# Kernel optimization log

Hardware: AMD Instinct MI355X
Metric: run time of the kernel (lower is better)

## Reference

```python
import jax, jax.numpy as jnp
import numpy as np

S, B, D, H, OUT = 512, 200, 64, 256, 3  # B == window_len - 2 = 200
EPS = 1e-5


def setup_inputs() -> dict:
    key = jax.random.key(0)
    ks = jax.random.split(key, 16)
    f = lambda k, sh, s=0.05: jax.random.normal(k, sh, dtype=jnp.float32) * s
    return {
        "x": f(ks[0], (S, B, D), 1.0),
        "w_ih0": f(ks[1], (3 * H, D)), "w_hh0": f(ks[2], (3 * H, H)),
        "b_ih0": f(ks[3], (3 * H,)), "b_hh0": f(ks[4], (3 * H,)),
        "w_ih1": f(ks[5], (3 * H, H)), "w_hh1": f(ks[6], (3 * H, H)),
        "b_ih1": f(ks[7], (3 * H,)), "b_hh1": f(ks[8], (3 * H,)),
        "ln_w": jnp.ones((H,), jnp.float32), "ln_b": jnp.zeros((H,), jnp.float32),
        "fc2_w": f(ks[9], (512, B * H), 0.01), "fc2_b": f(ks[10], (512,)),
        "bn_g": jnp.ones((512,), jnp.float32), "bn_b": jnp.zeros((512,), jnp.float32),
        "fc3_w": f(ks[11], (OUT, 512)), "fc3_b": f(ks[12], (OUT,)),
    }


def _gru_layer(x, w_ih, w_hh, b_ih, b_hh):
    # x: (S, B, D_in) -> (S, B, H), torch nn.GRU gate order [r, z, n]
    gi = jnp.einsum('sbd,gd->sbg', x, w_ih) + b_ih  # precompute input gates
    h0 = jnp.zeros((x.shape[1], w_hh.shape[1]), x.dtype)

    def step(h, gi_t):
        gh = h @ w_hh.T + b_hh
        ir, iz, inn = jnp.split(gi_t, 3, axis=-1)
        hr, hz, hn = jnp.split(gh, 3, axis=-1)
        r = jax.nn.sigmoid(ir + hr)
        z = jax.nn.sigmoid(iz + hz)
        n = jnp.tanh(inn + r * hn)
        h_new = (1.0 - z) * n + z * h
        return h_new, h_new

    _, hs = jax.lax.scan(step, h0, gi)
    return hs


def reference(x, w_ih0, w_hh0, b_ih0, b_hh0, w_ih1, w_hh1, b_ih1, b_hh1,
              ln_w, ln_b, fc2_w, fc2_b, bn_g, bn_b, fc3_w, fc3_b):
    h = _gru_layer(x, w_ih0, w_hh0, b_ih0, b_hh0)
    h = _gru_layer(h, w_ih1, w_hh1, b_ih1, b_hh1)
    # LayerNorm over hidden dim, then ReLU
    mu = jnp.mean(h, axis=-1, keepdims=True)
    var = jnp.var(h, axis=-1, keepdims=True)
    h = (h - mu) * jax.lax.rsqrt(var + EPS) * ln_w + ln_b
    h = jax.nn.relu(h)
    # flatten: (S, B*H)
    h = h.reshape(h.shape[0], -1)
    y = h @ fc2_w.T + fc2_b
    # BatchNorm1d (training mode: batch stats over axis 0, biased var)
    mu2 = jnp.mean(y, axis=0)
    var2 = jnp.var(y, axis=0)
    y = (y - mu2) * jax.lax.rsqrt(var2 + EPS) * bn_g + bn_b
    y = jax.nn.relu(y)
    return y @ fc3_w.T + fc3_b
```

## Files before the change

### kernel.cpp

```cpp
#include <hip/hip_runtime.h>
#include <stdint.h>

typedef _Float16 f16;
typedef _Float16 f16x4 __attribute__((ext_vector_type(4)));
typedef _Float16 f16x8 __attribute__((ext_vector_type(8)));
typedef float f32x4 __attribute__((ext_vector_type(4)));

#define SEQ 512
#define NB  200
#define HD  256
#define GD  768
#define BW  16
#define NBLK 13
#define GI_TSTRIDE (NBLK*4*6*512)
#define LOG2E 1.44269504f

__device__ __forceinline__ f32x4 mfma16(f16x8 a, f16x8 b, f32x4 c){
  return __builtin_amdgcn_mfma_f32_16x16x32_f16(a, b, c, 0, 0, 0);
}

__global__ void cvt_f32_f16(const float* __restrict__ src, f16* __restrict__ dst, int n4){
  int i = blockIdx.x * blockDim.x + threadIdx.x;
  int stride = gridDim.x * blockDim.x;
  for (; i < n4; i += stride){
    float4 v = ((const float4*)src)[i];
    f16x4 o = { (f16)v.x, (f16)v.y, (f16)v.z, (f16)v.w };
    ((f16x4*)dst)[i] = o;
  }
}

template<int MODE>
__global__ __launch_bounds__(256, 2)
void gemm_bt(const f16* __restrict__ A, const f16* __restrict__ B,
             f16* __restrict__ Cb, float* __restrict__ Cf,
             const float* __restrict__ bias1, const float* __restrict__ bias2,
             int K, int N, int klen)
{
  const int l  = threadIdx.x & 63;
  const int w  = threadIdx.x >> 6;
  const int lr = l & 15, lg = l >> 4;
  const int Mb = blockIdx.x * 128 + (w >> 1) * 64;
  const int Nb = blockIdx.y * 128 + (w & 1) * 64;
  const int kb = blockIdx.z * klen;

  const f16* Ap = A + (size_t)(Mb + lr) * K + kb + lg * 8;
  const f16* Bp = B + (size_t)(Nb + lr) * K + kb + lg * 8;

  f32x4 acc[4][4];
  #pragma unroll
  for (int i = 0; i < 4; ++i)
    #pragma unroll
    for (int j = 0; j < 4; ++j)
      acc[i][j] = (f32x4){0.f, 0.f, 0.f, 0.f};

  for (int k = 0; k < klen; k += 32){
    f16x8 af[4], bfr[4];
    #pragma unroll
    for (int i = 0; i < 4; ++i){
      af[i]  = *(const f16x8*)(Ap + (size_t)i * 16 * K + k);
      bfr[i] = *(const f16x8*)(Bp + (size_t)i * 16 * K + k);
    }
    #pragma unroll
    for (int i = 0; i < 4; ++i)
      #pragma unroll
      for (int j = 0; j < 4; ++j)
        acc[i][j] = mfma16(af[i], bfr[j], acc[i][j]);
  }

  if (MODE == 0){
    float bv[4];
    #pragma unroll
    for (int j = 0; j < 4; ++j){
      int g = Nb + j*16 + lr;
      bv[j] = bias1[g] + (g < 512 ? bias2[g] : 0.f);
    }
    #pragma unroll
    for (int i = 0; i < 4; ++i)
      #pragma unroll
      for (int r = 0; r < 4; ++r){
        int row = Mb + i*16 + lg*4 + r;
        int t = (int)(((uint64_t)(uint32_t)row * 167773u) >> 25);
        int b = row - t*200;
        int bblk = b >> 4, blr = b & 15;
        #pragma unroll
        for (int j = 0; j < 4; ++j){
          int g = Nb + j*16 + lr;
          int q = g >> 8, jr = g & 255;
          int ww = jr >> 6, t4 = (jr >> 4) & 3, lg2 = (jr >> 2) & 3, rr = g & 3;
          size_t idx = ((((size_t)(t*13 + bblk)*4 + ww)*6 + (q*2 + (t4>>1)))*64
                        + lg2*16 + blr)*8 + (t4&1)*4 + rr;
          Cb[idx] = (f16)(acc[i][j][r] + bv[j]);
        }
      }
  } else {
    #pragma unroll
    for (int i = 0; i < 4; ++i)
      #pragma unroll
      for (int j = 0; j < 4; ++j)
        #pragma unroll
        for (int r = 0; r < 4; ++r){
          int row = Mb + i*16 + lg*4 + r;
          int col = Nb + j*16 + lr;
          Cf[((size_t)blockIdx.z * 512 + row) * N + col] = acc[i][j][r];
        }
  }
}

__global__
__attribute__((amdgpu_flat_work_group_size(256, 256), amdgpu_waves_per_eu(1, 1)))
void gru_layer(const f16* __restrict__ whh, const float* __restrict__ bhh,
               const f16* __restrict__ gi, f16* __restrict__ hs)
{
  __shared__ __align__(16) unsigned char sm[16384 + 49152 + 24576];
  const int tid = threadIdx.x;
  const int w  = tid >> 6, l = tid & 63;
  const int lr = l & 15, lg = l >> 4;
  const int b0 = blockIdx.x * BW;
  const bool bval = (b0 + lr) < NB;

  ((int4*)sm)[tid]       = make_int4(0,0,0,0);
  ((int4*)sm)[tid + 256] = make_int4(0,0,0,0);

  const f16* glane = gi + ((size_t)(blockIdx.x*4 + w))*6*512 + l*8;
#define DMA_GI(P) do { \
    _Pragma("unroll") \
    for (int c = 0; c < 6; ++c) \
      __builtin_amdgcn_global_load_lds( \
          (const __attribute__((address_space(1))) void*)(glane + c*512), \
          (__attribute__((address_space(3))) void*)(sm + 16384 + (P)*24576 + w*6144 + c*1024), \
          16, 0, 0); \
  } while(0)

  DMA_GI(0);

  f16x8 wA[12][8];
  #pragma unroll
  for (int q = 0; q < 3; ++q)
    #pragma unroll
    for (int t4 = 0; t4 < 4; ++t4)
      #pragma unroll
      for (int kk = 0; kk < 8; ++kk)
        wA[q*4+t4][kk] = *(const f16x8*)(whh + (size_t)(q*256 + w*64 + t4*16 + lr)*256 + kk*32 + lg*8);

  f16x4 bn[4];
  #pragma unroll
  for (int t4 = 0; t4 < 4; ++t4){
    float4 bv = *(const float4*)(bhh + 512 + w*64 + t4*16 + lg*4);
    bn[t4] = (f16x4){(f16)bv.x,(f16)bv.y,(f16)bv.z,(f16)bv.w};
  }

  const int cswz = ((lr ^ (lr >> 2)) & 3) << 4;
  const int hrd = lr*64 + ((lg*16) ^ cswz);
  const int girdb = 16384 + w*6144 + l*16;

  f16* hp = hs + (size_t)(b0 + lr)*HD + w*64 + lg*4;
  f16x4 hvp[4];
  #pragma unroll
  for (int t4 = 0; t4 < 4; ++t4) hvp[t4] = (f16x4){(f16)0.f,(f16)0.f,(f16)0.f,(f16)0.f};

  asm volatile("s_waitcnt vmcnt(0)" ::: "memory");
  __syncthreads();

#define GRUSTEP(P) do { \
    asm volatile("s_waitcnt vmcnt(4)" ::: "memory");  \
    f16x8 c0 = *(const f16x8*)(sm + (P)*24576 + girdb + 0*1024); \
    f16x8 c1 = *(const f16x8*)(sm + (P)*24576 + girdb + 1*1024); \
    f16x8 c2 = *(const f16x8*)(sm + (P)*24576 + girdb + 2*1024); \
    f16x8 c3 = *(const f16x8*)(sm + (P)*24576 + girdb + 3*1024); \
    f16x8 innA = *(const f16x8*)(sm + (P)*24576 + girdb + 4*1024); \
    f16x8 innB = *(const f16x8*)(sm + (P)*24576 + girdb + 5*1024); \
    f32x4 acc[12]; \
    _Pragma("unroll") \
    for (int t4 = 0; t4 < 4; ++t4){ \
      _Pragma("unroll") \
      for (int r = 0; r < 4; ++r){ \
        acc[0*4+t4][r] = (float)((t4 < 2 ? c0 : c1)[(t4&1)*4 + r]); \
        acc[1*4+t4][r] = (float)((t4 < 2 ? c2 : c3)[(t4&1)*4 + r]); \
        acc[2*4+t4][r] = (float)(bn[t4][r]); \
      } \
    } \
    glane += GI_TSTRIDE; \
    DMA_GI((P)^1); \
    _Pragma("unroll") \
    for (int kk = 0; kk < 8; ++kk){ \
      f16x8 hf = *(const f16x8*)(sm + (P)*8192 + kk*1024 + hrd); \
      _Pragma("unroll") \
      for (int i = 0; i < 12; ++i) \
        acc[i] = mfma16(wA[i][kk], hf, acc[i]); \
    } \
    _Pragma("unroll") \
    for (int t4 = 0; t4 < 4; ++t4){ \
      f16x4 hv; \
      _Pragma("unroll") \
      for (int r = 0; r < 4; ++r){ \
        float iv = (float)((t4 < 2 ? innA : innB)[(t4&1)*4 + r]); \
        float rg = __builtin_amdgcn_rcpf(1.f + __builtin_amdgcn_exp2f(-LOG2E*acc[0*4+t4][r])); \
        float zg = __builtin_amdgcn_rcpf(1.f + __builtin_amdgcn_exp2f(-LOG2E*acc[1*4+t4][r])); \
        float aa = iv + rg*acc[2*4+t4][r]; \
        float ng = 2.f*__builtin_amdgcn_rcpf(1.f + __builtin_amdgcn_exp2f(-2.f*LOG2E*aa)) - 1.f; \
        float h  = ng + zg*((float)hvp[t4][r] - ng); \
        hv[r] = (f16)h; \
      } \
      hvp[t4] = hv; \
      *(f16x4*)(sm + ((P)^1)*8192 \
                + (w*2 + (t4>>1))*1024 + lr*64 \
                + ((((t4&1)*32) | (lg*8)) ^ cswz)) = hv; \
      if (bval) *(f16x4*)(hp + t4*16) = hv; \
    } \
    hp += (size_t)NB*HD; \
    asm volatile("s_waitcnt lgkmcnt(0)" ::: "memory"); \
    __builtin_amdgcn_sched_barrier(0); \
    __builtin_amdgcn_s_barrier(); \
    __builtin_amdgcn_sched_barrier(0); \
  } while(0)

  for (int th = 0; th < SEQ/2; ++th){
    GRUSTEP(0);
    GRUSTEP(1);
  }
#undef GRUSTEP
#undef DMA_GI
}

__global__ __launch_bounds__(256)
void ln_relu(f16* __restrict__ hs, const float* __restrict__ lnw,
             const float* __restrict__ lnb)
{
  const int tid = threadIdx.x;
  const int wv = tid >> 6;
  const int lane = tid & 63;
  const int half = lane >> 5;
  const int c0 = (lane & 31) * 8;
  float gw[8], gb[8];
  #pragma unroll
  for (int r = 0; r < 8; ++r){ gw[r] = lnw[c0 + r]; gb[r] = lnb[c0 + r]; }
  const int npairs = SEQ * NB / 2;
  for (int pair = blockIdx.x * 4 + wv; pair < npairs; pair += gridDim.x * 4){
    f16* p = hs + (size_t)(pair*2 + half) * HD + c0;
    f16x8 v = *(const f16x8*)p;
    float f[8], s = 0.f, q = 0.f;
    #pragma unroll
    for (int r = 0; r < 8; ++r){ f[r] = (float)v[r]; s += f[r]; q += f[r]*f[r]; }
    #pragma unroll
    for (int off = 16; off; off >>= 1){
      s += __shfl_xor(s, off);
      q += __shfl_xor(q, off);
    }
    float mu = s * (1.f / HD);
    float var = q * (1.f / HD) - mu * mu;
    float rs = rsqrtf(var + 1e-5f);
    f16x8 o;
    #pragma unroll
    for (int r = 0; r < 8; ++r){
      float y = (f[r] - mu) * rs * gw[r] + gb[r];
      o[r] = (f16)fmaxf(y, 0.f);
    }
    *(f16x8*)p = o;
  }
}

__global__ __launch_bounds__(512)
void bn_relu(const float* __restrict__ part, const float* __restrict__ g,
             const float* __restrict__ b, float* __restrict__ z)
{
  __shared__ float lds[16];
  const int o = blockIdx.x, s = threadIdx.x, w = s >> 6;
  float y = 0.f;
  #pragma unroll
  for (int p = 0; p < 8; ++p) y += part[((size_t)p * 512 + o) * 512 + s];
  float su = y, q = y * y;
  #pragma unroll
  for (int off = 32; off; off >>= 1){
    su += __shfl_down(su, off);
    q  += __shfl_down(q, off);
  }
  if ((s & 63) == 0){ lds[w] = su; lds[8 + w] = q; }
  __syncthreads();
  float S = 0.f, Q = 0.f;
  #pragma unroll
  for (int i = 0; i < 8; ++i){ S += lds[i]; Q += lds[8 + i]; }
  float mu = S * (1.f / 512.f);
  float var = Q * (1.f / 512.f) - mu * mu;
  float zz = fmaxf((y - mu) * rsqrtf(var + 1e-5f) * g[o] + b[o], 0.f);
  z[(size_t)o * 512 + s] = zz;
}

__global__ __launch_bounds__(256)
void fc3_k(const float* __restrict__ z, const float* __restrict__ w,
           const float* __restrict__ b, float* __restrict__ out)
{
  __shared__ float lds[12];
  const int s = blockIdx.x, tid = threadIdx.x, wv = tid >> 6;
  float a0 = 0.f, a1 = 0.f, a2 = 0.f;
  for (int o = tid; o < 512; o += 256){
    float zz = z[(size_t)o * 512 + s];
    a0 += zz * w[o];
    a1 += zz * w[512 + o];
    a2 += zz * w[1024 + o];
  }
  #pragma unroll
  for (int off = 32; off; off >>= 1){
    a0 += __shfl_down(a0, off);
    a1 += __shfl_down(a1, off);
    a2 += __shfl_down(a2, off);
  }
  if ((tid & 63) == 0){ lds[wv] = a0; lds[4 + wv] = a1; lds[8 + wv] = a2; }
  __syncthreads();
  if (tid == 0){
    out[s*3 + 0] = lds[0] + lds[1] + lds[2]  + lds[3]  + b[0];
    out[s*3 + 1] = lds[4] + lds[5] + lds[6]  + lds[7]  + b[1];
    out[s*3 + 2] = lds[8] + lds[9] + lds[10] + lds[11] + b[2];
  }
}

extern "C" void kernel_launch(void* const* d_in, const int* in_sizes, int n_in,
                              void* d_out, int out_size, void* d_ws, size_t ws_size,
                              hipStream_t stream)
{
  (void)in_sizes; (void)n_in; (void)out_size; (void)ws_size;
  const float* x    = (const float*)d_in[0];
  const float* wih0 = (const float*)d_in[1];
  const float* whh0 = (const float*)d_in[2];
  const float* bih0 = (const float*)d_in[3];
  const float* bhh0 = (const float*)d_in[4];
  const float* wih1 = (const float*)d_in[5];
  const float* whh1 = (const float*)d_in[6];
  const float* bih1 = (const float*)d_in[7];
  const float* bhh1 = (const float*)d_in[8];
  const float* lnw  = (const float*)d_in[9];
  const float* lnb  = (const float*)d_in[10];
  const float* fc2w = (const float*)d_in[11];
  const float* bng  = (const float*)d_in[13];
  const float* bnb  = (const float*)d_in[14];
  const float* fc3w = (const float*)d_in[15];
  const float* fc3b = (const float*)d_in[16];
  float* out = (float*)d_out;

  char* ws = (char*)d_ws;
  size_t off = 0;
  auto alloc = [&](size_t bytes) -> void* {
    void* p = ws + off; off += (bytes + 255) & ~(size_t)255; return p;
  };
  f16* GI     = (f16*)alloc((size_t)SEQ*GI_TSTRIDE*2);
  f16* X16    = (f16*)alloc((size_t)SEQ*NB*64*2);
  f16* WI0    = (f16*)alloc((size_t)768*64*2);
  f16* WH0    = (f16*)alloc((size_t)768*256*2);
  f16* WI1    = (f16*)alloc((size_t)768*256*2);
  f16* WH1    = (f16*)alloc((size_t)768*256*2);
  f16* HS0    = (f16*)alloc((size_t)SEQ*NB*256*2);
  f16* HS1    = (f16*)alloc((size_t)SEQ*NB*256*2);
  float* PART = (float*)alloc((size_t)8*512*512*4);
  float* Z    = (float*)alloc((size_t)512*512*4);
  f16* FC2W   = GI;

  cvt_f32_f16<<<2048,256,0,stream>>>(x,    X16,  SEQ*NB*64/4);
  cvt_f32_f16<<<64,  256,0,stream>>>(wih0, WI0,  768*64/4);
  cvt_f32_f16<<<192, 256,0,stream>>>(whh0, WH0,  768*256/4);
  cvt_f32_f16<<<192, 256,0,stream>>>(wih1, WI1,  768*256/4);
  cvt_f32_f16<<<192, 256,0,stream>>>(whh1, WH1,  768*256/4);

  dim3 g0(800, 6, 1);
  gemm_bt<0><<<g0, 256, 0, stream>>>(X16, WI0, GI, nullptr, bih0, bhh0, 64, GD, 64);
  gru_layer<<<NBLK, 256, 0, stream>>>(WH0, bhh0, GI, HS0);
  gemm_bt<0><<<g0, 256, 0, stream>>>(HS0, WI1, GI, nullptr, bih1, bhh1, 256, GD, 256);
  gru_layer<<<NBLK, 256, 0, stream>>>(WH1, bhh1, GI, HS1);
  ln_relu<<<3200, 256, 0, stream>>>(HS1, lnw, lnb);
  cvt_f32_f16<<<4096,256,0,stream>>>(fc2w, FC2W, 512*51200/4);
  dim3 g2(4, 4, 8);
  gemm_bt<1><<<g2, 256, 0, stream>>>(FC2W, HS1, nullptr, PART, nullptr, nullptr, 51200, 512, 6400);
  bn_relu<<<512, 512, 0, stream>>>(PART, bng, bnb, Z);
  fc3_k<<<512, 256, 0, stream>>>(Z, fc3w, fc3b, out);
}
```

Before: 3.288 ms.

## Split GRU recurrent step across 16 waves per block instead of 4

```diff
diff --git a/kernel.cpp b/kernel.cpp
--- a/kernel.cpp
+++ b/kernel.cpp
@@ -12,7 +12,7 @@
 #define GD  768
 #define BW  16
 #define NBLK 13
-#define GI_TSTRIDE (NBLK*4*6*512)
+#define GI_TSTRIDE (NBLK*12288)
 #define LOG2E 1.44269504f
 
 __device__ __forceinline__ f32x4 mfma16(f16x8 a, f16x8 b, f32x4 c){
@@ -82,13 +82,16 @@
         int t = (int)(((uint64_t)(uint32_t)row * 167773u) >> 25);
         int b = row - t*200;
         int bblk = b >> 4, blr = b & 15;
+        size_t region = ((size_t)t*NBLK + bblk) * 12288;
         #pragma unroll
         for (int j = 0; j < 4; ++j){
           int g = Nb + j*16 + lr;
-          int q = g >> 8, jr = g & 255;
-          int ww = jr >> 6, t4 = (jr >> 4) & 3, lg2 = (jr >> 2) & 3, rr = g & 3;
-          size_t idx = ((((size_t)(t*13 + bblk)*4 + ww)*6 + (q*2 + (t4>>1)))*64
-                        + lg2*16 + blr)*8 + (t4&1)*4 + rr;
+          int q = g >> 8, jj = g & 255;
+          int ww = jj >> 4, jr = jj & 15;
+          int lane = (jr >> 2)*16 + blr;
+          size_t idx;
+          if (q < 2) idx = region + (size_t)ww*512 + lane*8 + q*4 + (jr & 3);
+          else       idx = region + (size_t)(16 + (ww>>1))*512 + (ww&1)*256 + lane*4 + (jr & 3);
           Cb[idx] = (f16)(acc[i][j][r] + bv[j]);
         }
       }
@@ -107,106 +110,87 @@
 }
 
 __global__
-__attribute__((amdgpu_flat_work_group_size(256, 256), amdgpu_waves_per_eu(1, 1)))
+__attribute__((amdgpu_flat_work_group_size(1024, 1024)))
 void gru_layer(const f16* __restrict__ whh, const float* __restrict__ bhh,
                const f16* __restrict__ gi, f16* __restrict__ hs)
 {
-  __shared__ __align__(16) unsigned char sm[16384 + 49152 + 24576];
+  __shared__ __align__(16) unsigned char sm[16384 + 49152 + 32768];
   const int tid = threadIdx.x;
   const int w  = tid >> 6, l = tid & 63;
   const int lr = l & 15, lg = l >> 4;
   const int b0 = blockIdx.x * BW;
   const bool bval = (b0 + lr) < NB;
 
-  ((int4*)sm)[tid]       = make_int4(0,0,0,0);
-  ((int4*)sm)[tid + 256] = make_int4(0,0,0,0);
-
-  const f16* glane = gi + ((size_t)(blockIdx.x*4 + w))*6*512 + l*8;
+  ((int2*)sm)[tid] = make_int2(0,0);
+
+  const int nchunk = 16 + (w >> 1);
+  const f16* glane = gi + (size_t)blockIdx.x * 12288 + l*8;
 #define DMA_GI(P) do { \
-    _Pragma("unroll") \
-    for (int c = 0; c < 6; ++c) \
-      __builtin_amdgcn_global_load_lds( \
-          (const __attribute__((address_space(1))) void*)(glane + c*512), \
-          (__attribute__((address_space(3))) void*)(sm + 16384 + (P)*24576 + w*6144 + c*1024), \
-          16, 0, 0); \
+    __builtin_amdgcn_global_load_lds( \
+        (const __attribute__((address_space(1))) void*)(glane + w*512), \
+        (__attribute__((address_space(3))) void*)(sm + 16384 + (P)*24576 + w*1024), \
+        16, 0, 0); \
+    __builtin_amdgcn_global_load_lds( \
+        (const __attribute__((address_space(1))) void*)(glane + nchunk*512), \
+        (__attribute__((address_space(3))) void*)(sm + 16384 + (P)*24576 + nchunk*1024), \
+        16, 0, 0); \
   } while(0)
 
   DMA_GI(0);
 
-  f16x8 wA[12][8];
+  f16x8 wA[3][8];
   #pragma unroll
   for (int q = 0; q < 3; ++q)
     #pragma unroll
-    for (int t4 = 0; t4 < 4; ++t4)
-      #pragma unroll
-      for (int kk = 0; kk < 8; ++kk)
-        wA[q*4+t4][kk] = *(const f16x8*)(whh + (size_t)(q*256 + w*64 + t4*16 + lr)*256 + kk*32 + lg*8);
-
-  f16x4 bn[4];
-  #pragma unroll
-  for (int t4 = 0; t4 < 4; ++t4){
-    float4 bv = *(const float4*)(bhh + 512 + w*64 + t4*16 + lg*4);
-    bn[t4] = (f16x4){(f16)bv.x,(f16)bv.y,(f16)bv.z,(f16)bv.w};
+    for (int kk = 0; kk < 8; ++kk)
+      wA[q][kk] = *(const f16x8*)(whh + (size_t)(q*256 + w*16 + lr)*256 + kk*32 + lg*8);
+
+  f16x4 bnv;
+  {
+    float4 bv = *(const float4*)(bhh + 512 + w*16 + lg*4);
+    bnv = (f16x4){(f16)bv.x,(f16)bv.y,(f16)bv.z,(f16)bv.w};
   }
 
   const int cswz = ((lr ^ (lr >> 2)) & 3) << 4;
-  const int hrd = lr*64 + ((lg*16) ^ cswz);
-  const int girdb = 16384 + w*6144 + l*16;
-
-  f16* hp = hs + (size_t)(b0 + lr)*HD + w*64 + lg*4;
-  f16x4 hvp[4];
-  #pragma unroll
-  for (int t4 = 0; t4 < 4; ++t4) hvp[t4] = (f16x4){(f16)0.f,(f16)0.f,(f16)0.f,(f16)0.f};
+  const int hrd  = lr*64 + ((lg*16) ^ cswz);
+  const int girz = 16384 + w*1024 + l*16;
+  const int gin  = 16384 + nchunk*1024 + (w&1)*512 + l*8;
+  const int hwb  = (w>>1)*1024 + lr*64 + ((((w&1)*32) + lg*8) ^ cswz);
+
+  f16* hp = hs + (size_t)(b0 + lr)*HD + w*16 + lg*4;
+  f16x4 hvp = (f16x4){(f16)0.f,(f16)0.f,(f16)0.f,(f16)0.f};
 
   asm volatile("s_waitcnt vmcnt(0)" ::: "memory");
   __syncthreads();
 
 #define GRUSTEP(P) do { \
-    asm volatile("s_waitcnt vmcnt(4)" ::: "memory");  \
-    f16x8 c0 = *(const f16x8*)(sm + (P)*24576 + girdb + 0*1024); \
-    f16x8 c1 = *(const f16x8*)(sm + (P)*24576 + girdb + 1*1024); \
-    f16x8 c2 = *(const f16x8*)(sm + (P)*24576 + girdb + 2*1024); \
-    f16x8 c3 = *(const f16x8*)(sm + (P)*24576 + girdb + 3*1024); \
-    f16x8 innA = *(const f16x8*)(sm + (P)*24576 + girdb + 4*1024); \
-    f16x8 innB = *(const f16x8*)(sm + (P)*24576 + girdb + 5*1024); \
-    f32x4 acc[12]; \
-    _Pragma("unroll") \
-    for (int t4 = 0; t4 < 4; ++t4){ \
-      _Pragma("unroll") \
-      for (int r = 0; r < 4; ++r){ \
-        acc[0*4+t4][r] = (float)((t4 < 2 ? c0 : c1)[(t4&1)*4 + r]); \
-        acc[1*4+t4][r] = (float)((t4 < 2 ? c2 : c3)[(t4&1)*4 + r]); \
-        acc[2*4+t4][r] = (float)(bn[t4][r]); \
-      } \
-    } \
+    asm volatile("s_waitcnt vmcnt(0)" ::: "memory");  \
+    f16x8 rz = *(const f16x8*)(sm + (P)*24576 + girz); \
+    f16x4 nn = *(const f16x4*)(sm + (P)*24576 + gin); \
+    f32x4 a0 = {0.f,0.f,0.f,0.f}, a1 = {0.f,0.f,0.f,0.f}; \
+    f32x4 a2 = {(float)bnv[0],(float)bnv[1],(float)bnv[2],(float)bnv[3]}; \
     glane += GI_TSTRIDE; \
     DMA_GI((P)^1); \
     _Pragma("unroll") \
     for (int kk = 0; kk < 8; ++kk){ \
       f16x8 hf = *(const f16x8*)(sm + (P)*8192 + kk*1024 + hrd); \
-      _Pragma("unroll") \
-      for (int i = 0; i < 12; ++i) \
-        acc[i] = mfma16(wA[i][kk], hf, acc[i]); \
+      a0 = mfma16(wA[0][kk], hf, a0); \
+      a1 = mfma16(wA[1][kk], hf, a1); \
+      a2 = mfma16(wA[2][kk], hf, a2); \
     } \
+    f16x4 hv; \
     _Pragma("unroll") \
-    for (int t4 = 0; t4 < 4; ++t4){ \
-      f16x4 hv; \
-      _Pragma("unroll") \
-      for (int r = 0; r < 4; ++r){ \
-        float iv = (float)((t4 < 2 ? innA : innB)[(t4&1)*4 + r]); \
-        float rg = __builtin_amdgcn_rcpf(1.f + __builtin_amdgcn_exp2f(-LOG2E*acc[0*4+t4][r])); \
-        float zg = __builtin_amdgcn_rcpf(1.f + __builtin_amdgcn_exp2f(-LOG2E*acc[1*4+t4][r])); \
-        float aa = iv + rg*acc[2*4+t4][r]; \
-        float ng = 2.f*__builtin_amdgcn_rcpf(1.f + __builtin_amdgcn_exp2f(-2.f*LOG2E*aa)) - 1.f; \
-        float h  = ng + zg*((float)hvp[t4][r] - ng); \
-        hv[r] = (f16)h; \
-      } \
-      hvp[t4] = hv; \
-      *(f16x4*)(sm + ((P)^1)*8192 \
-                + (w*2 + (t4>>1))*1024 + lr*64 \
-                + ((((t4&1)*32) | (lg*8)) ^ cswz)) = hv; \
-      if (bval) *(f16x4*)(hp + t4*16) = hv; \
+    for (int r = 0; r < 4; ++r){ \
+      float rg = __builtin_amdgcn_rcpf(1.f + __builtin_amdgcn_exp2f(-LOG2E*((float)rz[r] + a0[r]))); \
+      float zg = __builtin_amdgcn_rcpf(1.f + __builtin_amdgcn_exp2f(-LOG2E*((float)rz[4+r] + a1[r]))); \
+      float aa = (float)nn[r] + rg*a2[r]; \
+      float ng = 2.f*__builtin_amdgcn_rcpf(1.f + __builtin_amdgcn_exp2f(-2.f*LOG2E*aa)) - 1.f; \
+      float h  = ng + zg*((float)hvp[r] - ng); \
+      hv[r] = (f16)h; \
     } \
+    hvp = hv; \
+    *(f16x4*)(sm + ((P)^1)*8192 + hwb) = hv; \
+    if (bval) *(f16x4*)hp = hv; \
     hp += (size_t)NB*HD; \
     asm volatile("s_waitcnt lgkmcnt(0)" ::: "memory"); \
     __builtin_amdgcn_sched_barrier(0); \
@@ -361,9 +345,9 @@
 
   dim3 g0(800, 6, 1);
   gemm_bt<0><<<g0, 256, 0, stream>>>(X16, WI0, GI, nullptr, bih0, bhh0, 64, GD, 64);
-  gru_layer<<<NBLK, 256, 0, stream>>>(WH0, bhh0, GI, HS0);
+  gru_layer<<<NBLK, 1024, 0, stream>>>(WH0, bhh0, GI, HS0);
   gemm_bt<0><<<g0, 256, 0, stream>>>(HS0, WI1, GI, nullptr, bih1, bhh1, 256, GD, 256);
-  gru_layer<<<NBLK, 256, 0, stream>>>(WH1, bhh1, GI, HS1);
+  gru_layer<<<NBLK, 1024, 0, stream>>>(WH1, bhh1, GI, HS1);
   ln_relu<<<3200, 256, 0, stream>>>(HS1, lnw, lnb);
   cvt_f32_f16<<<4096,256,0,stream>>>(fc2w, FC2W, 512*51200/4);
   dim3 g2(4, 4, 8);
```

Result: slower. 3.706 ms (+12.7%).
